# Kernel optimization log

Hardware: AMD Instinct MI355X
Metric: run time of the kernel (lower is better)

The kernel has to match this reference:

```python
import jax, jax.numpy as jnp
import numpy as np

N_WORDS = 8192   # total words in batch (flattened ragged loop)
CHAR_LEN = 16    # chars per word (padded/fixed instance)
WORD_VOCAB = 50000
CHAR_VOCAB = 128
WORD_DIM = 300
CHAR_DIM = 64
CHAR_HID = 128   # per-direction LSTM hidden
INPUT_DIM = 512
INFO_DIM = WORD_DIM + 2 * CHAR_HID  # 556


def setup_inputs() -> dict:
    key = jax.random.key(0)
    ks = jax.random.split(key, 16)
    s_ih = 1.0 / np.sqrt(CHAR_DIM)
    s_hh = 1.0 / np.sqrt(CHAR_HID)
    s_out = 1.0 / np.sqrt(INFO_DIM)
    return {
        "word_ids": jax.random.randint(ks[0], (N_WORDS,), 0, WORD_VOCAB),
        "char_ids": jax.random.randint(ks[1], (N_WORDS, CHAR_LEN), 0, CHAR_VOCAB),
        "word_table": jax.random.normal(ks[2], (WORD_VOCAB, WORD_DIM), jnp.float32),
        "char_table": jax.random.normal(ks[3], (CHAR_VOCAB, CHAR_DIM), jnp.float32),
        "Wih_f": jax.random.uniform(ks[4], (4 * CHAR_HID, CHAR_DIM), jnp.float32, -s_ih, s_ih),
        "Whh_f": jax.random.uniform(ks[5], (4 * CHAR_HID, CHAR_HID), jnp.float32, -s_hh, s_hh),
        "bih_f": jax.random.uniform(ks[6], (4 * CHAR_HID,), jnp.float32, -s_hh, s_hh),
        "bhh_f": jax.random.uniform(ks[7], (4 * CHAR_HID,), jnp.float32, -s_hh, s_hh),
        "Wih_b": jax.random.uniform(ks[8], (4 * CHAR_HID, CHAR_DIM), jnp.float32, -s_ih, s_ih),
        "Whh_b": jax.random.uniform(ks[9], (4 * CHAR_HID, CHAR_HID), jnp.float32, -s_hh, s_hh),
        "bih_b": jax.random.uniform(ks[10], (4 * CHAR_HID,), jnp.float32, -s_hh, s_hh),
        "bhh_b": jax.random.uniform(ks[11], (4 * CHAR_HID,), jnp.float32, -s_hh, s_hh),
        "W_out": jax.random.uniform(ks[12], (INPUT_DIM, INFO_DIM), jnp.float32, -s_out, s_out),
        "b_out": jax.random.uniform(ks[13], (INPUT_DIM,), jnp.float32, -s_out, s_out),
    }


def _lstm_dir(x, Wih, Whh, bih, bhh, reverse):
    # x: [L, N, D] -> outputs [L, N, H]; PyTorch gate order i,f,g,o; zero init state.
    L, N, _ = x.shape
    H = Whh.shape[1]
    b = bih + bhh

    def step(carry, xt):
        h, c = carry
        gates = xt @ Wih.T + h @ Whh.T + b  # [N, 4H]
        i, f, g, o = jnp.split(gates, 4, axis=-1)
        c = jax.nn.sigmoid(f) * c + jax.nn.sigmoid(i) * jnp.tanh(g)
        h = jax.nn.sigmoid(o) * jnp.tanh(c)
        return (h, c), h

    init = (jnp.zeros((N, H), x.dtype), jnp.zeros((N, H), x.dtype))
    _, hs = jax.lax.scan(step, init, x, reverse=reverse)
    return hs


def reference(word_ids, char_ids, word_table, char_table,
              Wih_f, Whh_f, bih_f, bhh_f,
              Wih_b, Whh_b, bih_b, bhh_b,
              W_out, b_out):
    w = word_table[word_ids]                     # [N, WORD_DIM]
    ce = char_table[char_ids]                    # [N, L, CHAR_DIM]
    x = jnp.transpose(ce, (1, 0, 2))             # [L, N, CHAR_DIM]
    hf = _lstm_dir(x, Wih_f, Whh_f, bih_f, bhh_f, reverse=False)  # [L, N, H]
    hb = _lstm_dir(x, Wih_b, Whh_b, bih_b, bhh_b, reverse=True)   # [L, N, H]
    # torch.sum over char positions of bidirectional outputs
    char_feat = jnp.sum(jnp.concatenate([hf, hb], axis=-1), axis=0)  # [N, 2H]
    feat = jnp.concatenate([w, char_feat], axis=-1)                  # [N, INFO_DIM]
    return jnp.tanh(feat @ W_out.T + b_out)                          # [N, INPUT_DIM]
```

## Files before the change

kernel.cpp:

```cpp
#include <hip/hip_runtime.h>
#include <hip/hip_bf16.h>

typedef __bf16 bf16x8 __attribute__((ext_vector_type(8)));
typedef float  f32x4  __attribute__((ext_vector_type(4)));
typedef int    i32x4  __attribute__((ext_vector_type(4)));

#define N_WORDS   8192
#define CHAR_LEN  16
#define WORD_DIM  300
#define CHAR_DIM  64
#define HID       128
#define G4        512
#define INFO      556
#define KPAD      576
#define OUTD      512
#define WBL       32
#define WBO       32
#define L2E       1.4426950408889634f

__device__ __forceinline__ float tanh_(float x) {
    return 1.0f - 2.0f * __builtin_amdgcn_rcpf(1.0f + __builtin_amdgcn_exp2f((2.0f * L2E) * x));
}

__global__ void prep_kernel(const float* __restrict__ char_table,
                            const float* __restrict__ Wih_f, const float* __restrict__ bih_f,
                            const float* __restrict__ bhh_f,
                            const float* __restrict__ Wih_b, const float* __restrict__ bih_b,
                            const float* __restrict__ bhh_b,
                            const float* __restrict__ W_out,
                            const float* __restrict__ Whh_f, const float* __restrict__ Whh_b,
                            float* __restrict__ preT,
                            __bf16* __restrict__ Wpad, __bf16* __restrict__ WhhB) {
    __shared__ float x[CHAR_DIM];
    if (blockIdx.x < 256) {
        const int dir = blockIdx.x & 1;
        const int cid = blockIdx.x >> 1;
        const float* Wih = dir ? Wih_b : Wih_f;
        const float* b1  = dir ? bih_b : bih_f;
        const float* b2  = dir ? bhh_b : bhh_f;
        if (threadIdx.x < CHAR_DIM) x[threadIdx.x] = char_table[cid * CHAR_DIM + threadIdx.x];
        __syncthreads();
        for (int g = threadIdx.x; g < G4; g += 256) {
            const f32x4* w4 = (const f32x4*)(Wih + g * CHAR_DIM);
            const f32x4* x4 = (const f32x4*)x;
            float s = b1[g] + b2[g];
            #pragma unroll
            for (int d = 0; d < CHAR_DIM / 4; ++d) {
                f32x4 wv = w4[d], xv = x4[d];
                s += wv[0]*xv[0] + wv[1]*xv[1] + wv[2]*xv[2] + wv[3]*xv[3];
            }
            int tt = g >> 7, j = g & (HID - 1);
            float sc = (tt == 2) ? (-2.0f * L2E) : (-L2E);
            preT[(dir * 128 + cid) * G4 + j * 4 + tt] = s * sc;
        }
    } else {
        int idx = (blockIdx.x - 256) * 256 + threadIdx.x;
        if (idx < OUTD * KPAD) {
            int row = idx / KPAD, col = idx - row * KPAD;
            Wpad[idx] = (col < INFO) ? (__bf16)W_out[row * INFO + col] : (__bf16)0.0f;
        } else {
            int j = idx - OUTD * KPAD;
            if (j < 2 * G4 * HID) {
                const float* src = (j < G4 * HID) ? Whh_f : Whh_b;
                int k = (j < G4 * HID) ? j : j - G4 * HID;
                int gate = (k >> 14) & 3;
                float sc = (gate == 2) ? (-2.0f * L2E) : (-L2E);
                WhhB[j] = (__bf16)(src[k] * sc);
            }
        }
    }
}

__global__ __launch_bounds__(512, 2) void lstm_kernel(
        const int*   __restrict__ char_ids,
        const float* __restrict__ preT,
        const __bf16* __restrict__ WhhB,
        __bf16* __restrict__ char_feat) {
    const int dir = blockIdx.y;
    const int wb  = blockIdx.x * WBL;
    const __bf16* Whh = WhhB + dir * G4 * HID;
    const float* preD = preT + dir * 128 * G4;

    const int tid  = threadIdx.x;
    const int wave = tid >> 6;
    const int lane = tid & 63;
    const int col  = lane & 15;
    const int quad = lane >> 4;
    const int jbase = wave * 16;

    __shared__ __bf16 h_lds[2][WBL][136];
    __shared__ int    cidT[CHAR_LEN][WBL];

    {
        int w = tid >> 4, t = tid & 15;
        cidT[t][w] = char_ids[(wb + w) * CHAR_LEN + t] * (G4 * 4);
    }

    bf16x8 Bfrag[4][4];
    #pragma unroll
    for (int tt = 0; tt < 4; ++tt) {
        int row = tt * HID + jbase + col;
        #pragma unroll
        for (int ks = 0; ks < 4; ++ks)
            Bfrag[tt][ks] = *(const bf16x8*)(Whh + row * HID + ks * 32 + quad * 8);
    }

    const char* base_lane = (const char*)(preD + (jbase + col) * 4);

    f32x4 nx0[4], nx1[4], acc0[4], acc1[4];
    float c0[4] = {}, c1[4] = {}, s0[4] = {}, s1[4] = {};

    auto pref = [&](f32x4* nx, int g, int t) {
        const int tc = dir ? (CHAR_LEN - 1 - t) : t;
        i32x4 off = *(const i32x4*)(&cidT[tc][g * 16 + quad * 4]);
        #pragma unroll
        for (int r = 0; r < 4; ++r)
            nx[r] = *(const f32x4*)(base_lane + off[r]);
    };
    auto accinit = [&](f32x4* acc, const f32x4* nx) {
        #pragma unroll
        for (int tt = 0; tt < 4; ++tt)
            acc[tt] = (f32x4){nx[0][tt], nx[1][tt], nx[2][tt], nx[3][tt]};
    };
    auto mfmag = [&](f32x4* acc, int g, int buf) {
        const __bf16 (*hc)[136] = h_lds[buf];
        #pragma unroll
        for (int ks = 0; ks < 4; ++ks) {
            bf16x8 A = *(const bf16x8*)(&hc[g * 16 + col][ks * 32 + quad * 8]);
            #pragma unroll
            for (int tt = 0; tt < 4; ++tt)
                acc[tt] = __builtin_amdgcn_mfma_f32_16x16x32_bf16(A, Bfrag[tt][ks], acc[tt], 0, 0, 0);
        }
    };
    auto gates = [&](f32x4* acc, float* c, float* sh, int g, int buf, bool wr) {
        __bf16 (*hn)[136] = h_lds[buf];
        #pragma unroll
        for (int r = 0; r < 4; ++r) {
            float ti = __builtin_amdgcn_exp2f(acc[0][r]);
            float tf = __builtin_amdgcn_exp2f(acc[1][r]);
            float tg = __builtin_amdgcn_exp2f(fminf(acc[2][r], 38.0f));
            float to = __builtin_amdgcn_exp2f(acc[3][r]);
            float sf = __builtin_amdgcn_rcpf(1.0f + tf);
            float ig = (1.0f - tg) * __builtin_amdgcn_rcpf((1.0f + ti) * (1.0f + tg));
            float cv = sf * c[r] + ig;
            c[r] = cv;
            float tc2 = __builtin_amdgcn_exp2f(cv * (-2.0f * L2E));
            float hv = (1.0f - tc2) * __builtin_amdgcn_rcpf((1.0f + to) * (1.0f + tc2));
            sh[r] += hv;
            if (wr) hn[g * 16 + quad * 4 + r][jbase + col] = (__bf16)hv;
        }
    };

    __syncthreads();

    pref(nx0, 0, 0);
    pref(nx1, 1, 0);
    accinit(acc0, nx0);
    pref(nx0, 0, 1);
    accinit(acc1, nx1);
    gates(acc0, c0, s0, 0, 0, true);
    __syncthreads();

    for (int t = 1; t < CHAR_LEN; ++t) {
        accinit(acc0, nx0);
        mfmag(acc0, 0, (t - 1) & 1);
        pref(nx1, 1, t);
        gates(acc1, c1, s1, 1, (t - 1) & 1, true);
        __syncthreads();
        accinit(acc1, nx1);
        mfmag(acc1, 1, (t - 1) & 1);
        if (t + 1 < CHAR_LEN) pref(nx0, 0, t + 1);
        gates(acc0, c0, s0, 0, t & 1, t + 1 < CHAR_LEN);
        __syncthreads();
    }
    gates(acc1, c1, s1, 1, 0, false);

    #pragma unroll
    for (int r = 0; r < 4; ++r) {
        char_feat[(wb + quad * 4 + r) * 256 + dir * HID + jbase + col]      = (__bf16)s0[r];
        char_feat[(wb + 16 + quad * 4 + r) * 256 + dir * HID + jbase + col] = (__bf16)s1[r];
    }
}

__global__ __launch_bounds__(1024, 4) void out_kernel(
        const int*   __restrict__ word_ids,
        const float* __restrict__ word_table,
        const __bf16* __restrict__ char_feat,
        const __bf16* __restrict__ Wpad,
        const float* __restrict__ b_out,
        float* __restrict__ out) {
    const int wb  = blockIdx.x * WBO;
    const int tid = threadIdx.x;
    const int wave = tid >> 6, lane = tid & 63, col = lane & 15, quad = lane >> 4;
    const int nbase = wave * 32;

    __shared__ __bf16 feat[WBO][584];
    __shared__ int wid[WBO];
    if (tid < WBO) wid[tid] = word_ids[wb + tid];
    __syncthreads();
    for (int idx = tid; idx < WBO * 75; idx += 1024) {
        int row = idx / 75, ch = idx - row * 75;
        f32x4 v = *(const f32x4*)(word_table + wid[row] * WORD_DIM + ch * 4);
        __bf16* d = &feat[row][ch * 4];
        d[0] = (__bf16)v[0]; d[1] = (__bf16)v[1]; d[2] = (__bf16)v[2]; d[3] = (__bf16)v[3];
    }
    {
        int row = tid >> 5, ch = tid & 31;
        bf16x8 v = *(const bf16x8*)(char_feat + (wb + row) * 256 + ch * 8);
        __bf16* d = &feat[row][WORD_DIM + ch * 8];
        #pragma unroll
        for (int e = 0; e < 8; ++e) d[e] = v[e];
    }
    if (tid < WBO * 28) {
        int row = tid / 28, cc = tid - row * 28;
        feat[row][INFO + cc] = (__bf16)0.0f;
    }
    __syncthreads();

    f32x4 acc[2][2];
    #pragma unroll
    for (int mt = 0; mt < 2; ++mt)
        #pragma unroll
        for (int nt = 0; nt < 2; ++nt) acc[mt][nt] = (f32x4){0.f, 0.f, 0.f, 0.f};

    const __bf16* Wp0 = Wpad + (nbase + col) * KPAD;
    const __bf16* Wp1 = Wpad + (nbase + 16 + col) * KPAD;

    #pragma unroll 2
    for (int kb = 0; kb < KPAD / 32; ++kb) {
        const int ko = kb * 32 + quad * 8;
        bf16x8 B0 = *(const bf16x8*)(Wp0 + ko);
        bf16x8 B1 = *(const bf16x8*)(Wp1 + ko);
        bf16x8 A0 = *(const bf16x8*)(&feat[col][ko]);
        bf16x8 A1 = *(const bf16x8*)(&feat[16 + col][ko]);
        acc[0][0] = __builtin_amdgcn_mfma_f32_16x16x32_bf16(A0, B0, acc[0][0], 0, 0, 0);
        acc[1][0] = __builtin_amdgcn_mfma_f32_16x16x32_bf16(A1, B0, acc[1][0], 0, 0, 0);
        acc[0][1] = __builtin_amdgcn_mfma_f32_16x16x32_bf16(A0, B1, acc[0][1], 0, 0, 0);
        acc[1][1] = __builtin_amdgcn_mfma_f32_16x16x32_bf16(A1, B1, acc[1][1], 0, 0, 0);
    }

    #pragma unroll
    for (int nt = 0; nt < 2; ++nt) {
        int n = nbase + nt * 16 + col;
        float bo = b_out[n];
        #pragma unroll
        for (int mt = 0; mt < 2; ++mt)
            #pragma unroll
            for (int r = 0; r < 4; ++r) {
                int word = wb + mt * 16 + quad * 4 + r;
                out[word * OUTD + n] = tanh_(acc[mt][nt][r] + bo);
            }
    }
}

extern "C" void kernel_launch(void* const* d_in, const int* in_sizes, int n_in,
                              void* d_out, int out_size, void* d_ws, size_t ws_size,
                              hipStream_t stream) {
    const int*   word_ids   = (const int*)d_in[0];
    const int*   char_ids   = (const int*)d_in[1];
    const float* word_table = (const float*)d_in[2];
    const float* char_table = (const float*)d_in[3];
    const float* Wih_f = (const float*)d_in[4];
    const float* Whh_f = (const float*)d_in[5];
    const float* bih_f = (const float*)d_in[6];
    const float* bhh_f = (const float*)d_in[7];
    const float* Wih_b = (const float*)d_in[8];
    const float* Whh_b = (const float*)d_in[9];
    const float* bih_b = (const float*)d_in[10];
    const float* bhh_b = (const float*)d_in[11];
    const float* W_out = (const float*)d_in[12];
    const float* b_out = (const float*)d_in[13];

    char* ws = (char*)d_ws;
    float*  preT      = (float*)ws;
    __bf16* WhhB      = (__bf16*)(ws + 524288);
    __bf16* Wpad      = (__bf16*)(ws + 524288 + 262144);
    __bf16* char_feat = (__bf16*)(ws + 524288 + 262144 + 589824);

    prep_kernel<<<256 + (OUTD * KPAD + 2 * G4 * HID + 255) / 256, 256, 0, stream>>>(
        char_table, Wih_f, bih_f, bhh_f, Wih_b, bih_b, bhh_b,
        W_out, Whh_f, Whh_b, preT, Wpad, WhhB);
    lstm_kernel<<<dim3(N_WORDS / WBL, 2), 512, 0, stream>>>(char_ids, preT, WhhB, char_feat);
    out_kernel<<<N_WORDS / WBO, 1024, 0, stream>>>(word_ids, word_table, char_feat, Wpad, b_out,
                                                   (float*)d_out);
}
```

Before: 202.4 us.

## Shrink LSTM word block to one 16-word group and raise occupancy

Halves the number of words per LSTM block from 32 to 16, removing the two interleaved word groups that hid MFMA latency behind gate math. The block now runs a single dependency chain per step, with more blocks launched and launch bounds raised to 4 blocks per CU so that latency is hidden across resident blocks rather than inside one. This reduces registers and LDS per block but doubles the number of blocks, each loading the full Whh fragments.

```diff
diff --git a/kernel.cpp b/kernel.cpp
--- a/kernel.cpp
+++ b/kernel.cpp
@@ -14,7 +14,7 @@
 #define INFO      556
 #define KPAD      576
 #define OUTD      512
-#define WBL       32
+#define WBL       16
 #define WBO       32
 #define L2E       1.4426950408889634f
 
@@ -71,7 +71,7 @@
     }
 }
 
-__global__ __launch_bounds__(512, 2) void lstm_kernel(
+__global__ __launch_bounds__(512, 4) void lstm_kernel(
         const int*   __restrict__ char_ids,
         const float* __restrict__ preT,
         const __bf16* __restrict__ WhhB,
@@ -91,7 +91,7 @@
     __shared__ __bf16 h_lds[2][WBL][136];
     __shared__ int    cidT[CHAR_LEN][WBL];
 
-    {
+    if (tid < CHAR_LEN * WBL) {
         int w = tid >> 4, t = tid & 15;
         cidT[t][w] = char_ids[(wb + w) * CHAR_LEN + t] * (G4 * 4);
     }
@@ -107,32 +107,32 @@
 
     const char* base_lane = (const char*)(preD + (jbase + col) * 4);
 
-    f32x4 nx0[4], nx1[4], acc0[4], acc1[4];
-    float c0[4] = {}, c1[4] = {}, s0[4] = {}, s1[4] = {};
-
-    auto pref = [&](f32x4* nx, int g, int t) {
+    f32x4 nx[4], acc[4];
+    float c[4] = {}, s[4] = {};
+
+    auto pref = [&](int t) {
         const int tc = dir ? (CHAR_LEN - 1 - t) : t;
-        i32x4 off = *(const i32x4*)(&cidT[tc][g * 16 + quad * 4]);
+        i32x4 off = *(const i32x4*)(&cidT[tc][quad * 4]);
         #pragma unroll
         for (int r = 0; r < 4; ++r)
             nx[r] = *(const f32x4*)(base_lane + off[r]);
     };
-    auto accinit = [&](f32x4* acc, const f32x4* nx) {
+    auto accinit = [&]() {
         #pragma unroll
         for (int tt = 0; tt < 4; ++tt)
             acc[tt] = (f32x4){nx[0][tt], nx[1][tt], nx[2][tt], nx[3][tt]};
     };
-    auto mfmag = [&](f32x4* acc, int g, int buf) {
+    auto mfmag = [&](int buf) {
         const __bf16 (*hc)[136] = h_lds[buf];
         #pragma unroll
         for (int ks = 0; ks < 4; ++ks) {
-            bf16x8 A = *(const bf16x8*)(&hc[g * 16 + col][ks * 32 + quad * 8]);
+            bf16x8 A = *(const bf16x8*)(&hc[col][ks * 32 + quad * 8]);
             #pragma unroll
             for (int tt = 0; tt < 4; ++tt)
                 acc[tt] = __builtin_amdgcn_mfma_f32_16x16x32_bf16(A, Bfrag[tt][ks], acc[tt], 0, 0, 0);
         }
     };
-    auto gates = [&](f32x4* acc, float* c, float* sh, int g, int buf, bool wr) {
+    auto gates = [&](int buf, bool wr) {
         __bf16 (*hn)[136] = h_lds[buf];
         #pragma unroll
         for (int r = 0; r < 4; ++r) {
@@ -146,40 +146,40 @@
             c[r] = cv;
             float tc2 = __builtin_amdgcn_exp2f(cv * (-2.0f * L2E));
             float hv = (1.0f - tc2) * __builtin_amdgcn_rcpf((1.0f + to) * (1.0f + tc2));
-            sh[r] += hv;
-            if (wr) hn[g * 16 + quad * 4 + r][jbase + col] = (__bf16)hv;
-        }
-    };
-
-    __syncthreads();
-
-    pref(nx0, 0, 0);
-    pref(nx1, 1, 0);
-    accinit(acc0, nx0);
-    pref(nx0, 0, 1);
-    accinit(acc1, nx1);
-    gates(acc0, c0, s0, 0, 0, true);
-    __syncthreads();
-
-    for (int t = 1; t < CHAR_LEN; ++t) {
-        accinit(acc0, nx0);
-        mfmag(acc0, 0, (t - 1) & 1);
-        pref(nx1, 1, t);
-        gates(acc1, c1, s1, 1, (t - 1) & 1, true);
+            s[r] += hv;
+            if (wr) hn[quad * 4 + r][jbase + col] = (__bf16)hv;
+        }
+    };
+
+    __syncthreads();
+
+    pref(0);
+    accinit();
+    pref(1);
+    gates(0, true);
+    __syncthreads();
+
+    #pragma unroll 1
+    for (int tb = 1; tb < CHAR_LEN - 1; tb += 2) {
+        accinit();
+        pref(tb + 1);
+        mfmag(0);
+        gates(1, true);
         __syncthreads();
-        accinit(acc1, nx1);
-        mfmag(acc1, 1, (t - 1) & 1);
-        if (t + 1 < CHAR_LEN) pref(nx0, 0, t + 1);
-        gates(acc0, c0, s0, 0, t & 1, t + 1 < CHAR_LEN);
+        accinit();
+        pref(tb + 2);
+        mfmag(1);
+        gates(0, true);
         __syncthreads();
     }
-    gates(acc1, c1, s1, 1, 0, false);
-
-    #pragma unroll
-    for (int r = 0; r < 4; ++r) {
-        char_feat[(wb + quad * 4 + r) * 256 + dir * HID + jbase + col]      = (__bf16)s0[r];
-        char_feat[(wb + 16 + quad * 4 + r) * 256 + dir * HID + jbase + col] = (__bf16)s1[r];
-    }
+
+    accinit();
+    mfmag(0);
+    gates(1, false);
+
+    #pragma unroll
+    for (int r = 0; r < 4; ++r)
+        char_feat[(wb + quad * 4 + r) * 256 + dir * HID + jbase + col] = (__bf16)s[r];
 }
 
 __global__ __launch_bounds__(1024, 4) void out_kernel(
```

Result: faster. 198.1 us (-2.1%).
